# Performance work log

Hardware: AMD Instinct MI355X
Metric: run time of the kernel (lower is better)

## Reference

```python
import jax, jax.numpy as jnp
import numpy as np

N_EXPERTS = 8
D_IN = 1024
D_OUT = 1024
BATCH = 4096


def setup_inputs() -> dict:
    key = jax.random.key(0)
    k_x, k_w, k_b, k_a = jax.random.split(key, 4)
    xs = jax.random.normal(k_x, (BATCH, D_IN), dtype=jnp.float32)
    mxs = jnp.arange(BATCH, dtype=jnp.int32)  # opaque per-sample metadata, passed through
    actions = jax.random.randint(k_a, (BATCH,), 0, N_EXPERTS, dtype=jnp.int64)
    # Expert parameters: each submodule is Linear(D_IN -> D_OUT)
    W = jax.random.normal(k_w, (N_EXPERTS, D_OUT, D_IN), dtype=jnp.float32) / np.sqrt(D_IN)
    b = jax.random.normal(k_b, (N_EXPERTS, D_OUT), dtype=jnp.float32) * 0.01
    return {"xs": xs, "mxs": mxs, "actions": actions, "W": W, "b": b}


def reference(xs, mxs, actions, W, b):
    # Original: per-sample python loop y_i = submodule[actions[i]](x_i); cat along batch.
    # Vectorized: compute all experts densely (E small), then select per-sample row.
    y_all = jnp.einsum("bj,eij->bei", xs, W) + b[None, :, :]  # [B, E, D_OUT]
    ys = jnp.take_along_axis(y_all, actions[:, None, None].astype(jnp.int32), axis=1)
    ys = jnp.squeeze(ys, axis=1)  # [B, D_OUT]
    return (ys, mxs, actions)
```

## Files before the change

kernel.cpp:

```cpp
#include <hip/hip_runtime.h>

#define BATCH 4096
#define D_IN 1024
#define D_OUT 1024
#define N_EXPERTS 8

#define TM 64
#define TN 128
#define TK 32
#define MAX_TILES 71

#define WS_PERM    0
#define WS_STARTS  4096
#define WS_TILE_E  4112
#define WS_TILE_M  4200
#define WS_NTILES  4288

typedef __attribute__((ext_vector_type(8))) short short8;
typedef __attribute__((ext_vector_type(4))) float f32x4;

__global__ __launch_bounds__(256) void group_kernel(
    const int* __restrict__ actions, const int* __restrict__ mxs,
    int* __restrict__ ws, float* __restrict__ out, int meta_mode) {
    __shared__ int h[256][N_EXPERTS];
    __shared__ int starts_s[N_EXPERTS];

    const int t = threadIdx.x;
    const int i0 = t * 16;
    int a_loc[16];
    int lc[N_EXPERTS];
#pragma unroll
    for (int e = 0; e < N_EXPERTS; ++e) lc[e] = 0;

    const int M = BATCH * D_OUT;
#pragma unroll
    for (int i = 0; i < 16; ++i) {
        const int a = actions[i0 + i];
        a_loc[i] = a;
        ++lc[a];
        if (meta_mode == 1) {
            out[M + i0 + i] = (float)mxs[i0 + i];
            out[M + BATCH + i0 + i] = (float)a;
        } else if (meta_mode == 2) {
            out[M + i0 + i] = (float)mxs[i0 + i];
            ((long long*)(out + M + BATCH))[i0 + i] = (long long)a;
        }
    }
#pragma unroll
    for (int e = 0; e < N_EXPERTS; ++e) h[t][e] = lc[e];
    __syncthreads();

    for (int d = 1; d < 256; d <<= 1) {
        int v[N_EXPERTS];
        const bool act = (t >= d);
        if (act) {
#pragma unroll
            for (int e = 0; e < N_EXPERTS; ++e) v[e] = h[t - d][e];
        }
        __syncthreads();
        if (act) {
#pragma unroll
            for (int e = 0; e < N_EXPERTS; ++e) h[t][e] += v[e];
        }
        __syncthreads();
    }

    if (t == 0) {
        int s = 0, nt = 0;
        for (int e = 0; e < N_EXPERTS; ++e) {
            const int c = h[255][e];
            starts_s[e] = s;
            ws[WS_STARTS + e] = s;
            for (int m0 = 0; m0 < c; m0 += TM) {
                ws[WS_TILE_E + nt] = e;
                ws[WS_TILE_M + nt] = m0;
                ++nt;
            }
            s += c;
        }
        ws[WS_STARTS + N_EXPERTS] = s;
        ws[WS_NTILES] = nt;
    }
    __syncthreads();

    int off[N_EXPERTS];
#pragma unroll
    for (int e = 0; e < N_EXPERTS; ++e)
        off[e] = starts_s[e] + h[t][e] - lc[e];
#pragma unroll
    for (int i = 0; i < 16; ++i) {
        const int a = a_loc[i];
        ws[WS_PERM + off[a]] = i0 + i;
        ++off[a];
    }
}

__device__ __forceinline__ void cvt8(const float4 a, const float4 b,
                                     short8& h, short8& l) {
    float f[8] = {a.x, a.y, a.z, a.w, b.x, b.y, b.z, b.w};
#pragma unroll
    for (int i = 0; i < 8; ++i) {
        const unsigned u = __float_as_uint(f[i]);
        h[i] = (short)(u >> 16);
        const float r = f[i] - __uint_as_float(u & 0xffff0000u);
        l[i] = (short)(__float_as_uint(r) >> 16);
    }
}

__global__ __launch_bounds__(256) void moe_gemm(
    const float* __restrict__ xs, const float* __restrict__ W,
    const float* __restrict__ bias, const int* __restrict__ ws,
    float* __restrict__ out)
{
    const int tix = blockIdx.y;
    if (tix >= ws[WS_NTILES]) return;
    const int e   = ws[WS_TILE_E + tix];
    const int m0  = ws[WS_TILE_M + tix];
    const int s0  = ws[WS_STARTS + e];
    const int cnt = ws[WS_STARTS + e + 1] - s0;
    const int n0  = blockIdx.x * TN;

    __shared__ short Ahi[TM * TK];
    __shared__ short Alo[TM * TK];
    __shared__ short Bhi[TN * TK];
    __shared__ short Blo[TN * TK];
    __shared__ int   rows_s[TM];

    const int t = threadIdx.x;
    if (t < TM) {
        const int r = m0 + t;
        rows_s[t] = (r < cnt) ? ws[WS_PERM + s0 + r] : -1;
    }
    __syncthreads();

    const int lane = t & 63;
    const int wave = t >> 6;
    const int wm = (wave & 1) * 32;
    const int wn = (wave >> 1) * 64;

    const float zf = 0.f;
    f32x4 acc[2][4];
#pragma unroll
    for (int mi = 0; mi < 2; ++mi)
#pragma unroll
        for (int nj = 0; nj < 4; ++nj)
            acc[mi][nj] = (f32x4){zf, zf, zf, zf};

    const float* Wb = W + (size_t)e * (D_OUT * (size_t)D_IN) + (size_t)n0 * D_IN;
    const int j  = t & 3;
    const int rr = t >> 2;
    const int arow = rows_s[rr];
    const float* aptr = (arow >= 0) ? (xs + (size_t)arow * D_IN + j * 8) : nullptr;
    const int aoff_st = (rr >> 4) * 512 + (j * 16 + (rr & 15)) * 8;

    for (int k0 = 0; k0 < D_IN; k0 += TK) {
        __syncthreads();
        {
            float4 v0 = make_float4(0.f, 0.f, 0.f, 0.f), v1 = v0;
            if (aptr) {
                v0 = *(const float4*)(aptr + k0);
                v1 = *(const float4*)(aptr + k0 + 4);
            }
            short8 h, l;
            cvt8(v0, v1, h, l);
            *(short8*)&Ahi[aoff_st] = h;
            *(short8*)&Alo[aoff_st] = l;
        }
#pragma unroll
        for (int i = 0; i < 2; ++i) {
            const int n   = i * 64 + rr;
            const int off = (n >> 4) * 512 + (j * 16 + (n & 15)) * 8;
            const float* q = Wb + (size_t)n * D_IN + k0 + j * 8;
            const float4 w0 = *(const float4*)q;
            const float4 w1 = *(const float4*)(q + 4);
            short8 h, l;
            cvt8(w0, w1, h, l);
            *(short8*)&Bhi[off] = h;
            *(short8*)&Blo[off] = l;
        }
        __syncthreads();

        short8 ah[2], al[2], bh[4], bl[4];
#pragma unroll
        for (int i2 = 0; i2 < 2; ++i2) {
            const int aoff = ((wm >> 4) + i2) * 512 + lane * 8;
            ah[i2] = *(const short8*)&Ahi[aoff];
            al[i2] = *(const short8*)&Alo[aoff];
        }
#pragma unroll
        for (int i2 = 0; i2 < 4; ++i2) {
            const int boff = ((wn >> 4) + i2) * 512 + lane * 8;
            bh[i2] = *(const short8*)&Bhi[boff];
            bl[i2] = *(const short8*)&Blo[boff];
        }
#pragma unroll
        for (int mi = 0; mi < 2; ++mi)
#pragma unroll
            for (int nj = 0; nj < 4; ++nj) {
                acc[mi][nj] = __builtin_amdgcn_mfma_f32_16x16x32_bf16(ah[mi], bh[nj], acc[mi][nj], 0, 0, 0);
                acc[mi][nj] = __builtin_amdgcn_mfma_f32_16x16x32_bf16(ah[mi], bl[nj], acc[mi][nj], 0, 0, 0);
                acc[mi][nj] = __builtin_amdgcn_mfma_f32_16x16x32_bf16(al[mi], bh[nj], acc[mi][nj], 0, 0, 0);
            }
    }

    const int cl = lane & 15;
    const int qd = lane >> 4;
    float bv[4];
#pragma unroll
    for (int nj = 0; nj < 4; ++nj)
        bv[nj] = bias[e * D_OUT + n0 + wn + nj * 16 + cl];
#pragma unroll
    for (int mi = 0; mi < 2; ++mi) {
#pragma unroll
        for (int reg = 0; reg < 4; ++reg) {
            const int mloc = wm + mi * 16 + qd * 4 + reg;
            const int r = rows_s[mloc];
            if (r >= 0) {
                float* orow = out + (size_t)r * D_OUT + n0 + wn + cl;
#pragma unroll
                for (int nj = 0; nj < 4; ++nj)
                    orow[nj * 16] = acc[mi][nj][reg] + bv[nj];
            }
        }
    }
}

extern "C" void kernel_launch(void* const* d_in, const int* in_sizes, int n_in,
                              void* d_out, int out_size, void* d_ws, size_t ws_size,
                              hipStream_t stream) {
    const float* xs      = (const float*)d_in[0];
    const int*   mxs     = (const int*)d_in[1];
    const int*   actions = (const int*)d_in[2];
    const float* W       = (const float*)d_in[3];
    const float* bias    = (const float*)d_in[4];
    float* out = (float*)d_out;
    int*   ws  = (int*)d_ws;

    const int metaOff = BATCH * D_OUT;
    int meta_mode = 0;
    if (out_size >= metaOff + 3 * BATCH) meta_mode = 2;
    else if (out_size >= metaOff + 2 * BATCH) meta_mode = 1;

    group_kernel<<<1, 256, 0, stream>>>(actions, mxs, ws, out, meta_mode);

    dim3 grid(D_OUT / TN, MAX_TILES, 1);
    moe_gemm<<<grid, 256, 0, stream>>>(xs, W, bias, ws, out);
}
```

Measured before the change: 160.0 us.

## Use 128-row tiles, split-K with atomic accumulation, and double-buffered LDS prefetch

Doubles the M tile to 128 rows so each wave computes a 64x64 block, which raises reuse of the W tile. It splits K into two halves whose partial sums are combined with float atomicAdd into an output that a new kernel zeroes first, and it switches to a flat 1D grid. Global loads for the next K step are prefetched into registers and written to a second LDS buffer while MFMAs run on the current one. The cost is an extra full-output zeroing pass, atomic traffic on the output, and more registers and LDS per block, which limits occupancy.

```diff
diff --git a/kernel.cpp b/kernel.cpp
--- a/kernel.cpp
+++ b/kernel.cpp
@@ -5,16 +5,19 @@
 #define D_OUT 1024
 #define N_EXPERTS 8
 
-#define TM 64
+#define TM 128
 #define TN 128
 #define TK 32
-#define MAX_TILES 71
+#define KSPLIT 2
+#define KHALF (D_IN / KSPLIT)
+#define NSTEPS (KHALF / TK)
+#define MAX_TILES 39
 
 #define WS_PERM    0
 #define WS_STARTS  4096
 #define WS_TILE_E  4112
-#define WS_TILE_M  4200
-#define WS_NTILES  4288
+#define WS_TILE_M  4160
+#define WS_NTILES  4224
 
 typedef __attribute__((ext_vector_type(8))) short short8;
 typedef __attribute__((ext_vector_type(4))) float f32x4;
@@ -95,6 +98,11 @@
     }
 }
 
+__global__ __launch_bounds__(256) void zero_kernel(float* __restrict__ out) {
+    const int i = blockIdx.x * 256 + threadIdx.x;
+    ((float4*)out)[i] = make_float4(0.f, 0.f, 0.f, 0.f);
+}
+
 __device__ __forceinline__ void cvt8(const float4 a, const float4 b,
                                      short8& h, short8& l) {
     float f[8] = {a.x, a.y, a.z, a.w, b.x, b.y, b.z, b.w};
@@ -107,100 +115,121 @@
     }
 }
 
-__global__ __launch_bounds__(256) void moe_gemm(
+__global__ __launch_bounds__(256, 2) void moe_gemm(
     const float* __restrict__ xs, const float* __restrict__ W,
     const float* __restrict__ bias, const int* __restrict__ ws,
     float* __restrict__ out)
 {
-    const int tix = blockIdx.y;
+    const int id  = blockIdx.x;
+    const int nx  = id & 7;
+    const int rem = id >> 3;
+    const int tix = rem % MAX_TILES;
+    const int kh  = rem / MAX_TILES;
     if (tix >= ws[WS_NTILES]) return;
     const int e   = ws[WS_TILE_E + tix];
     const int m0  = ws[WS_TILE_M + tix];
     const int s0  = ws[WS_STARTS + e];
     const int cnt = ws[WS_STARTS + e + 1] - s0;
-    const int n0  = blockIdx.x * TN;
-
-    __shared__ short Ahi[TM * TK];
-    __shared__ short Alo[TM * TK];
-    __shared__ short Bhi[TN * TK];
-    __shared__ short Blo[TN * TK];
-    __shared__ int   rows_s[TM];
+    const int n0  = nx * TN;
+    const int kbase = kh * KHALF;
+    const int* perm = ws + WS_PERM + s0 + m0;
+    const int rem_rows = cnt - m0;
+
+    __shared__ short Ahi[2][TM * TK];
+    __shared__ short Alo[2][TM * TK];
+    __shared__ short Bhi[2][TN * TK];
+    __shared__ short Blo[2][TN * TK];
 
     const int t = threadIdx.x;
-    if (t < TM) {
-        const int r = m0 + t;
-        rows_s[t] = (r < cnt) ? ws[WS_PERM + s0 + r] : -1;
-    }
-    __syncthreads();
-
     const int lane = t & 63;
     const int wave = t >> 6;
-    const int wm = (wave & 1) * 32;
+    const int wm = (wave & 1) * 64;
     const int wn = (wave >> 1) * 64;
 
-    const float zf = 0.f;
-    f32x4 acc[2][4];
-#pragma unroll
-    for (int mi = 0; mi < 2; ++mi)
+    const float* apt[2];
+    const float* bpt[2];
+#pragma unroll
+    for (int i = 0; i < 2; ++i) {
+        const int c = t + i * 256;
+        const int row_l = ((c >> 6) << 4) | (c & 15);
+        const int kq = (c & 63) >> 4;
+        int ra = perm[(row_l < rem_rows) ? row_l : 0];
+        apt[i] = xs + (size_t)ra * D_IN + kbase + kq * 8;
+        bpt[i] = W + ((size_t)e << 20) + (size_t)(n0 + row_l) * D_IN + kbase + kq * 8;
+    }
+    const int st0 = t * 8;
+    const int st1 = (t + 256) * 8;
+
+    f32x4 acc[4][4];
+#pragma unroll
+    for (int mi = 0; mi < 4; ++mi)
 #pragma unroll
         for (int nj = 0; nj < 4; ++nj)
-            acc[mi][nj] = (f32x4){zf, zf, zf, zf};
-
-    const float* Wb = W + (size_t)e * (D_OUT * (size_t)D_IN) + (size_t)n0 * D_IN;
-    const int j  = t & 3;
-    const int rr = t >> 2;
-    const int arow = rows_s[rr];
-    const float* aptr = (arow >= 0) ? (xs + (size_t)arow * D_IN + j * 8) : nullptr;
-    const int aoff_st = (rr >> 4) * 512 + (j * 16 + (rr & 15)) * 8;
-
-    for (int k0 = 0; k0 < D_IN; k0 += TK) {
+            acc[mi][nj] = (f32x4){0.f, 0.f, 0.f, 0.f};
+
+    float4 pa[2][2], pb[2][2];
+#pragma unroll
+    for (int i = 0; i < 2; ++i) {
+        pa[i][0] = *(const float4*)(apt[i]);
+        pa[i][1] = *(const float4*)(apt[i] + 4);
+        pb[i][0] = *(const float4*)(bpt[i]);
+        pb[i][1] = *(const float4*)(bpt[i] + 4);
+    }
+    {
+        short8 h, l;
+        cvt8(pa[0][0], pa[0][1], h, l);
+        *(short8*)&Ahi[0][st0] = h; *(short8*)&Alo[0][st0] = l;
+        cvt8(pa[1][0], pa[1][1], h, l);
+        *(short8*)&Ahi[0][st1] = h; *(short8*)&Alo[0][st1] = l;
+        cvt8(pb[0][0], pb[0][1], h, l);
+        *(short8*)&Bhi[0][st0] = h; *(short8*)&Blo[0][st0] = l;
+        cvt8(pb[1][0], pb[1][1], h, l);
+        *(short8*)&Bhi[0][st1] = h; *(short8*)&Blo[0][st1] = l;
+    }
+
+    for (int s = 0; s < NSTEPS; ++s) {
+        const int cur = s & 1;
         __syncthreads();
-        {
-            float4 v0 = make_float4(0.f, 0.f, 0.f, 0.f), v1 = v0;
-            if (aptr) {
-                v0 = *(const float4*)(aptr + k0);
-                v1 = *(const float4*)(aptr + k0 + 4);
-            }
-            short8 h, l;
-            cvt8(v0, v1, h, l);
-            *(short8*)&Ahi[aoff_st] = h;
-            *(short8*)&Alo[aoff_st] = l;
-        }
-#pragma unroll
-        for (int i = 0; i < 2; ++i) {
-            const int n   = i * 64 + rr;
-            const int off = (n >> 4) * 512 + (j * 16 + (n & 15)) * 8;
-            const float* q = Wb + (size_t)n * D_IN + k0 + j * 8;
-            const float4 w0 = *(const float4*)q;
-            const float4 w1 = *(const float4*)(q + 4);
-            short8 h, l;
-            cvt8(w0, w1, h, l);
-            *(short8*)&Bhi[off] = h;
-            *(short8*)&Blo[off] = l;
-        }
-        __syncthreads();
-
-        short8 ah[2], al[2], bh[4], bl[4];
-#pragma unroll
-        for (int i2 = 0; i2 < 2; ++i2) {
+        if (s + 1 < NSTEPS) {
+            const int ko = (s + 1) * TK;
+#pragma unroll
+            for (int i = 0; i < 2; ++i) {
+                pa[i][0] = *(const float4*)(apt[i] + ko);
+                pa[i][1] = *(const float4*)(apt[i] + ko + 4);
+                pb[i][0] = *(const float4*)(bpt[i] + ko);
+                pb[i][1] = *(const float4*)(bpt[i] + ko + 4);
+            }
+        }
+        short8 ah[4], al[4], bh[4], bl[4];
+#pragma unroll
+        for (int i2 = 0; i2 < 4; ++i2) {
             const int aoff = ((wm >> 4) + i2) * 512 + lane * 8;
-            ah[i2] = *(const short8*)&Ahi[aoff];
-            al[i2] = *(const short8*)&Alo[aoff];
-        }
-#pragma unroll
-        for (int i2 = 0; i2 < 4; ++i2) {
+            ah[i2] = *(const short8*)&Ahi[cur][aoff];
+            al[i2] = *(const short8*)&Alo[cur][aoff];
             const int boff = ((wn >> 4) + i2) * 512 + lane * 8;
-            bh[i2] = *(const short8*)&Bhi[boff];
-            bl[i2] = *(const short8*)&Blo[boff];
-        }
-#pragma unroll
-        for (int mi = 0; mi < 2; ++mi)
+            bh[i2] = *(const short8*)&Bhi[cur][boff];
+            bl[i2] = *(const short8*)&Blo[cur][boff];
+        }
+#pragma unroll
+        for (int mi = 0; mi < 4; ++mi)
 #pragma unroll
             for (int nj = 0; nj < 4; ++nj) {
                 acc[mi][nj] = __builtin_amdgcn_mfma_f32_16x16x32_bf16(ah[mi], bh[nj], acc[mi][nj], 0, 0, 0);
                 acc[mi][nj] = __builtin_amdgcn_mfma_f32_16x16x32_bf16(ah[mi], bl[nj], acc[mi][nj], 0, 0, 0);
                 acc[mi][nj] = __builtin_amdgcn_mfma_f32_16x16x32_bf16(al[mi], bh[nj], acc[mi][nj], 0, 0, 0);
             }
+        if (s + 1 < NSTEPS) {
+            const int nxt = cur ^ 1;
+            short8 h, l;
+            cvt8(pa[0][0], pa[0][1], h, l);
+            *(short8*)&Ahi[nxt][st0] = h; *(short8*)&Alo[nxt][st0] = l;
+            cvt8(pa[1][0], pa[1][1], h, l);
+            *(short8*)&Ahi[nxt][st1] = h; *(short8*)&Alo[nxt][st1] = l;
+            cvt8(pb[0][0], pb[0][1], h, l);
+            *(short8*)&Bhi[nxt][st0] = h; *(short8*)&Blo[nxt][st0] = l;
+            cvt8(pb[1][0], pb[1][1], h, l);
+            *(short8*)&Bhi[nxt][st1] = h; *(short8*)&Blo[nxt][st1] = l;
+        }
     }
 
     const int cl = lane & 15;
@@ -208,18 +237,18 @@
     float bv[4];
 #pragma unroll
     for (int nj = 0; nj < 4; ++nj)
-        bv[nj] = bias[e * D_OUT + n0 + wn + nj * 16 + cl];
-#pragma unroll
-    for (int mi = 0; mi < 2; ++mi) {
+        bv[nj] = (kh == 0) ? bias[e * D_OUT + n0 + wn + nj * 16 + cl] : 0.f;
+#pragma unroll
+    for (int mi = 0; mi < 4; ++mi) {
 #pragma unroll
         for (int reg = 0; reg < 4; ++reg) {
-            const int mloc = wm + mi * 16 + qd * 4 + reg;
-            const int r = rows_s[mloc];
-            if (r >= 0) {
+            const int row_l = wm + mi * 16 + qd * 4 + reg;
+            if (row_l < rem_rows) {
+                const int r = perm[row_l];
                 float* orow = out + (size_t)r * D_OUT + n0 + wn + cl;
 #pragma unroll
                 for (int nj = 0; nj < 4; ++nj)
-                    orow[nj * 16] = acc[mi][nj][reg] + bv[nj];
+                    atomicAdd(&orow[nj * 16], acc[mi][nj][reg] + bv[nj]);
             }
         }
     }
@@ -241,8 +270,8 @@
     if (out_size >= metaOff + 3 * BATCH) meta_mode = 2;
     else if (out_size >= metaOff + 2 * BATCH) meta_mode = 1;
 
+    zero_kernel<<<(BATCH * D_OUT) / (256 * 4), 256, 0, stream>>>(out);
     group_kernel<<<1, 256, 0, stream>>>(actions, mxs, ws, out, meta_mode);
 
-    dim3 grid(D_OUT / TN, MAX_TILES, 1);
-    moe_gemm<<<grid, 256, 0, stream>>>(xs, W, bias, ws, out);
-}
+    moe_gemm<<<8 * MAX_TILES * KSPLIT, 256, 0, stream>>>(xs, W, bias, ws, out);
+}
```

New measurement: 191.9 us. +20.0%, slower.

## Split K across two blocks with atomic accumulation and simplify tile loads

Applied to the files above, without the earlier changes.

Splits the reduction dimension of the grouped expert GEMM in two, so twice as many blocks run, and each writes partial sums into the output with atomicAdd. The output is zeroed by a new kernel first, and only the first half adds the bias. The grid is flattened to 1D with n-tile-fastest ordering, and the row-index shared array with its sync is dropped in favour of reading the permutation directly. The load and LDS-store mapping is also rearranged. The cost is an extra zeroing pass over the 16MB output and doubled read-modify-write traffic from the float atomics.

```diff
diff --git a/kernel.cpp b/kernel.cpp
--- a/kernel.cpp
+++ b/kernel.cpp
@@ -8,6 +8,9 @@
 #define TM 64
 #define TN 128
 #define TK 32
+#define KSPLIT 2
+#define KHALF (D_IN / KSPLIT)
+#define NSTEPS (KHALF / TK)
 #define MAX_TILES 71
 
 #define WS_PERM    0
@@ -95,6 +98,11 @@
     }
 }
 
+__global__ __launch_bounds__(256) void zero_kernel(float* __restrict__ out) {
+    const int i = blockIdx.x * 256 + threadIdx.x;
+    ((float4*)out)[i] = make_float4(0.f, 0.f, 0.f, 0.f);
+}
+
 __device__ __forceinline__ void cvt8(const float4 a, const float4 b,
                                      short8& h, short8& l) {
     float f[8] = {a.x, a.y, a.z, a.w, b.x, b.y, b.z, b.w};
@@ -112,71 +120,73 @@
     const float* __restrict__ bias, const int* __restrict__ ws,
     float* __restrict__ out)
 {
-    const int tix = blockIdx.y;
+    const int id  = blockIdx.x;
+    const int nx  = id & 7;
+    const int rem = id >> 3;
+    const int tix = rem % MAX_TILES;
+    const int kh  = rem / MAX_TILES;
     if (tix >= ws[WS_NTILES]) return;
     const int e   = ws[WS_TILE_E + tix];
     const int m0  = ws[WS_TILE_M + tix];
     const int s0  = ws[WS_STARTS + e];
     const int cnt = ws[WS_STARTS + e + 1] - s0;
-    const int n0  = blockIdx.x * TN;
+    const int n0  = nx * TN;
+    const int kbase = kh * KHALF;
+    const int* perm = ws + WS_PERM + s0 + m0;
+    const int rem_rows = cnt - m0;
 
     __shared__ short Ahi[TM * TK];
     __shared__ short Alo[TM * TK];
     __shared__ short Bhi[TN * TK];
     __shared__ short Blo[TN * TK];
-    __shared__ int   rows_s[TM];
 
     const int t = threadIdx.x;
-    if (t < TM) {
-        const int r = m0 + t;
-        rows_s[t] = (r < cnt) ? ws[WS_PERM + s0 + r] : -1;
-    }
-    __syncthreads();
-
     const int lane = t & 63;
     const int wave = t >> 6;
     const int wm = (wave & 1) * 32;
     const int wn = (wave >> 1) * 64;
 
-    const float zf = 0.f;
+    const int arow_l = ((t >> 6) << 4) | (t & 15);
+    const int kq = (t >> 4) & 3;
+    const int ra = perm[(arow_l < rem_rows) ? arow_l : 0];
+    const float* ap = xs + (size_t)ra * D_IN + kbase + kq * 8;
+    const float* bp0;
+    const float* bp1;
+    {
+        const int c0 = t;
+        const int row0 = ((c0 >> 6) << 4) | (c0 & 15);
+        bp0 = W + ((size_t)e << 20) + (size_t)(n0 + row0) * D_IN + kbase + ((c0 >> 4) & 3) * 8;
+        const int c1 = t + 256;
+        const int row1 = ((c1 >> 6) << 4) | (c1 & 15);
+        bp1 = W + ((size_t)e << 20) + (size_t)(n0 + row1) * D_IN + kbase + ((c1 >> 4) & 3) * 8;
+    }
+    const int st0 = t * 8;
+    const int st1 = (t + 256) * 8;
+
     f32x4 acc[2][4];
 #pragma unroll
     for (int mi = 0; mi < 2; ++mi)
 #pragma unroll
         for (int nj = 0; nj < 4; ++nj)
-            acc[mi][nj] = (f32x4){zf, zf, zf, zf};
-
-    const float* Wb = W + (size_t)e * (D_OUT * (size_t)D_IN) + (size_t)n0 * D_IN;
-    const int j  = t & 3;
-    const int rr = t >> 2;
-    const int arow = rows_s[rr];
-    const float* aptr = (arow >= 0) ? (xs + (size_t)arow * D_IN + j * 8) : nullptr;
-    const int aoff_st = (rr >> 4) * 512 + (j * 16 + (rr & 15)) * 8;
-
-    for (int k0 = 0; k0 < D_IN; k0 += TK) {
+            acc[mi][nj] = (f32x4){0.f, 0.f, 0.f, 0.f};
+
+    for (int s = 0; s < NSTEPS; ++s) {
+        const int k0 = s * TK;
         __syncthreads();
         {
-            float4 v0 = make_float4(0.f, 0.f, 0.f, 0.f), v1 = v0;
-            if (aptr) {
-                v0 = *(const float4*)(aptr + k0);
-                v1 = *(const float4*)(aptr + k0 + 4);
-            }
+            const float4 a0 = *(const float4*)(ap + k0);
+            const float4 a1 = *(const float4*)(ap + k0 + 4);
+            const float4 b00 = *(const float4*)(bp0 + k0);
+            const float4 b01 = *(const float4*)(bp0 + k0 + 4);
+            const float4 b10 = *(const float4*)(bp1 + k0);
+            const float4 b11 = *(const float4*)(bp1 + k0 + 4);
             short8 h, l;
-            cvt8(v0, v1, h, l);
-            *(short8*)&Ahi[aoff_st] = h;
-            *(short8*)&Alo[aoff_st] = l;
-        }
-#pragma unroll
-        for (int i = 0; i < 2; ++i) {
-            const int n   = i * 64 + rr;
-            const int off = (n >> 4) * 512 + (j * 16 + (n & 15)) * 8;
-            const float* q = Wb + (size_t)n * D_IN + k0 + j * 8;
-            const float4 w0 = *(const float4*)q;
-            const float4 w1 = *(const float4*)(q + 4);
-            short8 h, l;
-            cvt8(w0, w1, h, l);
-            *(short8*)&Bhi[off] = h;
-            *(short8*)&Blo[off] = l;
+            cvt8(a0, a1, h, l);
+            *(short8*)&Ahi[st0] = h; *(short8*)&Alo[st0] = l;
+            cvt8(b00, b01, h, l);
+            *(short8*)&Bhi[st0] = h; *(short8*)&Blo[st0] = l;
+            cvt8(b10, b11, h, l);
+            *(short8*)&Bhi[st1] = h; *(short8*)&Blo[st1] = l;
         }
         __syncthreads();
 
@@ -208,18 +218,18 @@
     float bv[4];
 #pragma unroll
     for (int nj = 0; nj < 4; ++nj)
-        bv[nj] = bias[e * D_OUT + n0 + wn + nj * 16 + cl];
+        bv[nj] = (kh == 0) ? bias[e * D_OUT + n0 + wn + nj * 16 + cl] : 0.f;
 #pragma unroll
     for (int mi = 0; mi < 2; ++mi) {
 #pragma unroll
         for (int reg = 0; reg < 4; ++reg) {
-            const int mloc = wm + mi * 16 + qd * 4 + reg;
-            const int r = rows_s[mloc];
-            if (r >= 0) {
+            const int row_l = wm + mi * 16 + qd * 4 + reg;
+            if (row_l < rem_rows) {
+                const int r = perm[row_l];
                 float* orow = out + (size_t)r * D_OUT + n0 + wn + cl;
 #pragma unroll
                 for (int nj = 0; nj < 4; ++nj)
-                    orow[nj * 16] = acc[mi][nj][reg] + bv[nj];
+                    atomicAdd(&orow[nj * 16], acc[mi][nj][reg] + bv[nj]);
             }
         }
     }
@@ -241,8 +251,8 @@
     if (out_size >= metaOff + 3 * BATCH) meta_mode = 2;
     else if (out_size >= metaOff + 2 * BATCH) meta_mode = 1;
 
+    zero_kernel<<<(BATCH * D_OUT) / (256 * 4), 256, 0, stream>>>(out);
     group_kernel<<<1, 256, 0, stream>>>(actions, mxs, ws, out, meta_mode);
 
-    dim3 grid(D_OUT / TN, MAX_TILES, 1);
-    moe_gemm<<<grid, 256, 0, stream>>>(xs, W, bias, ws, out);
-}
+    moe_gemm<<<8 * MAX_TILES * KSPLIT, 256, 0, stream>>>(xs, W, bias, ws, out);
+}
```

Measured after the change: 184.3 us. 1.15x slower.
